# Performance work log

Hardware: AMD Instinct MI355X
Metric: run time of the kernel (lower is better)

Reference implementation:

```python
import jax, jax.numpy as jnp
import numpy as np

D_MODEL = 1024
NUM_HEADS = 16
D_K = D_MODEL // NUM_HEADS


def setup_inputs() -> dict:
    key = jax.random.key(0)
    ks = jax.random.split(key, 9)
    s = 1.0 / np.sqrt(D_MODEL)
    x = jax.random.normal(ks[0], (4, 2048, D_MODEL), dtype=jnp.float32)
    Wq = jax.random.uniform(ks[1], (D_MODEL, D_MODEL), jnp.float32, -s, s)
    bq = jax.random.uniform(ks[2], (D_MODEL,), jnp.float32, -s, s)
    Wk = jax.random.uniform(ks[3], (D_MODEL, D_MODEL), jnp.float32, -s, s)
    bk = jax.random.uniform(ks[4], (D_MODEL,), jnp.float32, -s, s)
    Wv = jax.random.uniform(ks[5], (D_MODEL, D_MODEL), jnp.float32, -s, s)
    bv = jax.random.uniform(ks[6], (D_MODEL,), jnp.float32, -s, s)
    Wo = jax.random.uniform(ks[7], (D_MODEL, D_MODEL), jnp.float32, -s, s)
    bo = jax.random.uniform(ks[8], (D_MODEL,), jnp.float32, -s, s)
    return {"x": x, "Wq": Wq, "bq": bq, "Wk": Wk, "bk": bk,
            "Wv": Wv, "bv": bv, "Wo": Wo, "bo": bo}


def reference(x, Wq, bq, Wk, bk, Wv, bv, Wo, bo):
    B, S, _ = x.shape
    # Linear projections (torch Linear: x @ W.T + b)
    q = x @ Wq.T + bq
    k = x @ Wk.T + bk
    v = x @ Wv.T + bv
    # [B, H, S, d_k]
    q = q.reshape(B, S, NUM_HEADS, D_K).transpose(0, 2, 1, 3)
    k = k.reshape(B, S, NUM_HEADS, D_K).transpose(0, 2, 1, 3)
    v = v.reshape(B, S, NUM_HEADS, D_K).transpose(0, 2, 1, 3)
    score = jnp.einsum('bhqd,bhkd->bhqk', q, k) / jnp.sqrt(jnp.float32(D_K))
    causal = jnp.tril(jnp.ones((S, S), dtype=bool))  # True = keep
    score = jnp.where(causal[None, None], score, -jnp.inf)
    attn = jax.nn.softmax(score, axis=-1)
    out = jnp.einsum('bhqk,bhkd->bhqd', attn, v)
    out = out.transpose(0, 2, 1, 3).reshape(B, S, D_MODEL)
    return out @ Wo.T + bo
```

## Files before the change

kernel.cpp:

```cpp
#include <hip/hip_runtime.h>
#include <hip/hip_bf16.h>
#include <stdint.h>

#define D_MODEL 1024
#define SEQ     2048
#define BATCH   4
#define NHEAD   16
#define DKH     64
#define MTOT    (BATCH * SEQ)

typedef __bf16 bf16x8 __attribute__((ext_vector_type(8)));
typedef __bf16 bf16x4 __attribute__((ext_vector_type(4)));
typedef float  floatx4 __attribute__((ext_vector_type(4)));
typedef short  s16x4  __attribute__((ext_vector_type(4)));

#define GLOAD_LDS16(gp, lp)                                            \
    __builtin_amdgcn_global_load_lds(                                  \
        (const __attribute__((address_space(1))) unsigned int*)(gp),   \
        (__attribute__((address_space(3))) unsigned int*)(lp), 16, 0, 0)

#define MFMA16(a, b, c) __builtin_amdgcn_mfma_f32_16x16x32_bf16(a, b, c, 0, 0, 0)

#if __has_builtin(__builtin_amdgcn_exp2f)
#define EXP2(x) __builtin_amdgcn_exp2f(x)
#else
#define EXP2(x) exp2f(x)
#endif

static __device__ __forceinline__ floatx4 pv_mfma(s16x4 a, s16x4 b, floatx4 c)
{
#if __has_builtin(__builtin_amdgcn_mfma_f32_16x16x16bf16_1k)
    return __builtin_amdgcn_mfma_f32_16x16x16bf16_1k(a, b, c, 0, 0, 0);
#else
    asm("v_mfma_f32_16x16x16_bf16 %0, %1, %2, %0" : "+v"(c) : "v"(a), "v"(b));
    return c;
#endif
}

__global__ __launch_bounds__(256)
void cvt_x_kernel(const float* __restrict__ src, __bf16* __restrict__ dst)
{
    const int i = (blockIdx.x * 256 + threadIdx.x) * 4;
    floatx4 v = *(const floatx4*)(src + i);
    bf16x4 o;
    o[0] = (__bf16)v[0]; o[1] = (__bf16)v[1]; o[2] = (__bf16)v[2]; o[3] = (__bf16)v[3];
    *(bf16x4*)(dst + i) = o;
}

__global__ __launch_bounds__(256)
void cvt_w3_kernel(const float* __restrict__ Wq, const float* __restrict__ Wk,
                   const float* __restrict__ Wv, __bf16* __restrict__ Wcat)
{
    const int z = blockIdx.y;
    const float* src = (z == 0) ? Wq : ((z == 1) ? Wk : Wv);
    const int i = (blockIdx.x * 256 + threadIdx.x) * 4;
    floatx4 v = *(const floatx4*)(src + i);
    bf16x4 o;
    o[0] = (__bf16)v[0]; o[1] = (__bf16)v[1]; o[2] = (__bf16)v[2]; o[3] = (__bf16)v[3];
    *(bf16x4*)(Wcat + (size_t)z * (D_MODEL * D_MODEL) + i) = o;
}

__global__ __launch_bounds__(256)
void qkv_gemm_kernel(const __bf16* __restrict__ xb, const __bf16* __restrict__ Wcat,
                     const float* __restrict__ bq, const float* __restrict__ bk,
                     const float* __restrict__ bv,
                     __bf16* __restrict__ Q, __bf16* __restrict__ K,
                     __bf16* __restrict__ Vt)
{
    __shared__ __align__(16) char smem_raw[128 * 136 * 2];
    __bf16* As = (__bf16*)smem_raw;
    __bf16* Bs = (__bf16*)(smem_raw + 8192);
    __bf16* Cs = (__bf16*)smem_raw;

    const int t    = threadIdx.x;
    const int w    = t >> 6, l = t & 63, quad = l >> 4, r16 = l & 15;
    const int wm   = w & 1, wn = w >> 1;
    const int m0   = blockIdx.y * 128;
    const int n0   = blockIdx.x * 128;
    const int z    = n0 >> 10;
    const float* bias = (z == 0) ? bq : ((z == 1) ? bk : bv);
    __bf16* outQK     = (z == 0) ? Q  : K;
    const float scale = (z == 0) ? 0.18033688011112042f : 1.0f;

    floatx4 acc[4][4];
#pragma unroll
    for (int i = 0; i < 4; ++i)
#pragma unroll
        for (int j = 0; j < 4; ++j) acc[i][j] = (floatx4){0.f, 0.f, 0.f, 0.f};

    const int c0 = t, c1 = t + 256;
    const __bf16* Ag0 = xb   + (size_t)(m0 + (c0 >> 2)) * 1024 + (c0 & 3) * 8;
    const __bf16* Ag1 = xb   + (size_t)(m0 + (c1 >> 2)) * 1024 + (c1 & 3) * 8;
    const __bf16* Bg0 = Wcat + (size_t)(n0 + (c0 >> 2)) * 1024 + (c0 & 3) * 8;
    const __bf16* Bg1 = Wcat + (size_t)(n0 + (c1 >> 2)) * 1024 + (c1 & 3) * 8;
    unsigned int* lAs = (unsigned int*)As;
    unsigned int* lBs = (unsigned int*)Bs;

    for (int k0 = 0; k0 < 1024; k0 += 32) {
        __syncthreads();
        GLOAD_LDS16(Ag0 + k0, lAs + c0 * 4);
        GLOAD_LDS16(Ag1 + k0, lAs + c1 * 4);
        GLOAD_LDS16(Bg0 + k0, lBs + c0 * 4);
        GLOAD_LDS16(Bg1 + k0, lBs + c1 * 4);
        __syncthreads();

        bf16x8 af[4], bfm[4];
#pragma unroll
        for (int i = 0; i < 4; ++i)
            af[i] = *(const bf16x8*)&As[(wm * 64 + i * 16 + r16) * 32 + quad * 8];
#pragma unroll
        for (int j = 0; j < 4; ++j)
            bfm[j] = *(const bf16x8*)&Bs[(wn * 64 + j * 16 + r16) * 32 + quad * 8];
#pragma unroll
        for (int i = 0; i < 4; ++i)
#pragma unroll
            for (int j = 0; j < 4; ++j)
                acc[i][j] = MFMA16(af[i], bfm[j], acc[i][j]);
    }

    __syncthreads();

    if (z == 2) {
#pragma unroll
        for (int i = 0; i < 4; ++i) {
            const int mb = wm * 64 + i * 16 + quad * 4;
#pragma unroll
            for (int j = 0; j < 4; ++j) {
                const int nl = wn * 64 + j * 16 + r16;
                const float bb = bias[(n0 + nl) & 1023];
                bf16x4 p4;
#pragma unroll
                for (int r = 0; r < 4; ++r) p4[r] = (__bf16)(acc[i][j][r] + bb);
                *(bf16x4*)&Cs[nl * 136 + mb] = p4;
            }
        }
    } else {
#pragma unroll
        for (int i = 0; i < 4; ++i) {
            const int mb = wm * 64 + i * 16 + quad * 4;
#pragma unroll
            for (int j = 0; j < 4; ++j) {
                const int nl = wn * 64 + j * 16 + r16;
                const float bb = bias[(n0 + nl) & 1023];
#pragma unroll
                for (int r = 0; r < 4; ++r)
                    Cs[(mb + r) * 136 + nl] =
                        (__bf16)((acc[i][j][r] + bb) * scale);
            }
        }
    }
    __syncthreads();

    const int b  = m0 >> 11;
    if (z == 2) {
#pragma unroll
        for (int k = 0; k < 8; ++k) {
            const int nl = (t >> 4) + k * 16;
            const int ml = (t & 15) * 8;
            bf16x8 row = *(const bf16x8*)&Cs[nl * 136 + ml];
            const int f = (n0 + nl) & 1023, h = f >> 6, d = f & 63;
            const int s = (m0 & 2047) + ml;
            *(bf16x8*)&Vt[((size_t)((b * 16 + h) * 64 + d) << 11) + s] = row;
        }
    } else {
#pragma unroll
        for (int k = 0; k < 8; ++k) {
            const int ml = (t >> 4) + k * 16;
            const int nl = (t & 15) * 8;
            bf16x8 row = *(const bf16x8*)&Cs[ml * 136 + nl];
            const int f = (n0 + nl) & 1023, h = f >> 6, d = f & 63;
            const int s = (m0 & 2047) + ml;
            *(bf16x8*)&outQK[((size_t)(b * 16 + h) << 17) + ((size_t)s << 6) + d]
                = row;
        }
    }
}

__global__ __launch_bounds__(256)
void out_gemm_kernel(const __bf16* __restrict__ A, const __bf16* __restrict__ Wob,
                     const float* __restrict__ bo, float* __restrict__ out)
{
    __shared__ __align__(16) __bf16 As[128 * 32];
    __shared__ __align__(16) __bf16 Bs[128 * 32];

    const int t    = threadIdx.x;
    const int w    = t >> 6, l = t & 63, quad = l >> 4, r16 = l & 15;
    const int wm   = w & 1, wn = w >> 1;
    const int m0   = blockIdx.y * 128;
    const int n0   = blockIdx.x * 128;

    floatx4 acc[4][4];
#pragma unroll
    for (int i = 0; i < 4; ++i)
#pragma unroll
        for (int j = 0; j < 4; ++j) acc[i][j] = (floatx4){0.f, 0.f, 0.f, 0.f};

    const int c0 = t, c1 = t + 256;
    const __bf16* Ag0 = A   + (size_t)(m0 + (c0 >> 2)) * 1024 + (c0 & 3) * 8;
    const __bf16* Ag1 = A   + (size_t)(m0 + (c1 >> 2)) * 1024 + (c1 & 3) * 8;
    const __bf16* Bg0 = Wob + (size_t)(n0 + (c0 >> 2)) * 1024 + (c0 & 3) * 8;
    const __bf16* Bg1 = Wob + (size_t)(n0 + (c1 >> 2)) * 1024 + (c1 & 3) * 8;
    unsigned int* lAs = (unsigned int*)As;
    unsigned int* lBs = (unsigned int*)Bs;

    for (int k0 = 0; k0 < 1024; k0 += 32) {
        __syncthreads();
        GLOAD_LDS16(Ag0 + k0, lAs + c0 * 4);
        GLOAD_LDS16(Ag1 + k0, lAs + c1 * 4);
        GLOAD_LDS16(Bg0 + k0, lBs + c0 * 4);
        GLOAD_LDS16(Bg1 + k0, lBs + c1 * 4);
        __syncthreads();

        bf16x8 af[4], bfm[4];
#pragma unroll
        for (int i = 0; i < 4; ++i)
            af[i] = *(const bf16x8*)&As[(wm * 64 + i * 16 + r16) * 32 + quad * 8];
#pragma unroll
        for (int j = 0; j < 4; ++j)
            bfm[j] = *(const bf16x8*)&Bs[(wn * 64 + j * 16 + r16) * 32 + quad * 8];
#pragma unroll
        for (int i = 0; i < 4; ++i)
#pragma unroll
            for (int j = 0; j < 4; ++j)
                acc[i][j] = MFMA16(af[i], bfm[j], acc[i][j]);
    }

#pragma unroll
    for (int i = 0; i < 4; ++i) {
        const int mg = m0 + wm * 64 + i * 16 + quad * 4;
#pragma unroll
        for (int j = 0; j < 4; ++j) {
            const int ng = n0 + wn * 64 + j * 16 + r16;
            const float bb = bo[ng];
#pragma unroll
            for (int r = 0; r < 4; ++r)
                out[(size_t)(mg + r) * 1024 + ng] = acc[i][j][r] + bb;
        }
    }
}

__global__ __launch_bounds__(256, 4)
void attn_kernel(const __bf16* __restrict__ Qg, const __bf16* __restrict__ Kg,
                 const __bf16* __restrict__ Vtg, __bf16* __restrict__ O)
{
    __shared__ __align__(16) __bf16 Ks[2][64 * 72];
    __shared__ __align__(16) __bf16 Vs[2][64 * 72];

    const int t    = threadIdx.x;
    const int w    = t >> 6, l = t & 63, quad = l >> 4, r16 = l & 15;
    const int bh   = blockIdx.x;
    const int y    = blockIdx.y;
    const int p    = y >> 1, half = y & 1;
    const int qa   = 15 - p, qb = p;
    const size_t base = (size_t)bh * SEQ * DKH;
    const int d0   = 2 * qa + half;
    const int d1   = 2 * qb + half;
    const int nkt  = d0 + 1;
    const int row0 = qa * 128 + half * 64 + w * 16;
    const int row1 = qb * 128 + half * 64 + w * 16;

    const s16x4 ones16 = {(short)0x3F80, (short)0x3F80,
                          (short)0x3F80, (short)0x3F80};

    bf16x8 qf00, qf01, qf10, qf11;
    qf00 = *(const bf16x8*)&Qg[base + (size_t)(row0 + r16) * 64 + quad * 8];
    qf01 = *(const bf16x8*)&Qg[base + (size_t)(row0 + r16) * 64 + 32 + quad * 8];
    qf10 = *(const bf16x8*)&Qg[base + (size_t)(row1 + r16) * 64 + quad * 8];
    qf11 = *(const bf16x8*)&Qg[base + (size_t)(row1 + r16) * 64 + 32 + quad * 8];

    floatx4 o[2][4];
#pragma unroll
    for (int mi = 0; mi < 2; ++mi)
#pragma unroll
        for (int j = 0; j < 4; ++j) o[mi][j] = (floatx4){0.f, 0.f, 0.f, 0.f};
    floatx4 osum[2];
    osum[0] = (floatx4){0.f, 0.f, 0.f, 0.f};
    osum[1] = (floatx4){0.f, 0.f, 0.f, 0.f};

    const int srow = t >> 3;
    const int sg   = (t & 7) * 8;

    bf16x8 kc0, kc1, vc0, vc1;
    kc0 = *(const bf16x8*)&Kg[base + (size_t)srow * 64 + sg];
    kc1 = *(const bf16x8*)&Kg[base + (size_t)(32 + srow) * 64 + sg];
    vc0 = *(const bf16x8*)&Vtg[base + (size_t)srow * 2048 + sg];
    vc1 = *(const bf16x8*)&Vtg[base + (size_t)(32 + srow) * 2048 + sg];

    for (int kt = 0; kt < nkt; ++kt) {
        __bf16* ks = Ks[kt & 1];
        __bf16* vs = Vs[kt & 1];
        *(bf16x8*)&ks[srow * 72 + sg] = kc0;
        *(bf16x8*)&ks[(32 + srow) * 72 + sg] = kc1;
        *(bf16x8*)&vs[srow * 72 + sg] = vc0;
        *(bf16x8*)&vs[(32 + srow) * 72 + sg] = vc1;
        if (kt + 1 < nkt) {
            const int kr = (kt + 1) * 64;
            kc0 = *(const bf16x8*)&Kg[base + (size_t)(kr + srow) * 64 + sg];
            kc1 = *(const bf16x8*)&Kg[base + (size_t)(kr + 32 + srow) * 64 + sg];
            vc0 = *(const bf16x8*)&Vtg[base + (size_t)srow * 2048 + kr + sg];
            vc1 = *(const bf16x8*)&Vtg[base + (size_t)(32 + srow) * 2048 + kr + sg];
        }
        __syncthreads();

        const bool a1 = (kt <= d1);
        __builtin_amdgcn_s_setprio(1);
        bf16x8 kf0, kf1;
#pragma unroll
        for (int j = 0; j < 4; ++j) {
            kf0 = *(const bf16x8*)&ks[(j * 16 + r16) * 72 + quad * 8];
            kf1 = *(const bf16x8*)&ks[(j * 16 + r16) * 72 + 32 + quad * 8];
            floatx4 z0 = (floatx4){0.f, 0.f, 0.f, 0.f};
            floatx4 z1 = (floatx4){0.f, 0.f, 0.f, 0.f};
            z0 = MFMA16(kf0, qf00, z0);
            z0 = MFMA16(kf1, qf01, z0);
            if (a1) {
                z1 = MFMA16(kf0, qf10, z1);
                z1 = MFMA16(kf1, qf11, z1);
            }
            const int kg = kt * 64 + j * 16 + quad * 4;
            bf16x4 pb0, pb1;
            if (kt < d0) {
#pragma unroll
                for (int r = 0; r < 4; ++r)
                    pb0[r] = (__bf16)EXP2(z0[r]);
            } else {
                const int qg0 = row0 + r16;
#pragma unroll
                for (int r = 0; r < 4; ++r) {
                    float pp = 0.f;
                    if (kg + r <= qg0) pp = EXP2(z0[r]);
                    pb0[r] = (__bf16)pp;
                }
            }
            s16x4 pa0 = __builtin_bit_cast(s16x4, pb0);
            s16x4 pa1;
            if (a1) {
                if (kt < d1) {
#pragma unroll
                    for (int r = 0; r < 4; ++r)
                        pb1[r] = (__bf16)EXP2(z1[r]);
                } else {
                    const int qg1 = row1 + r16;
#pragma unroll
                    for (int r = 0; r < 4; ++r) {
                        float pp = 0.f;
                        if (kg + r <= qg1) pp = EXP2(z1[r]);
                        pb1[r] = (__bf16)pp;
                    }
                }
                pa1 = __builtin_bit_cast(s16x4, pb1);
            }
            osum[0] = pv_mfma(pa0, ones16, osum[0]);
            if (a1) osum[1] = pv_mfma(pa1, ones16, osum[1]);
#pragma unroll
            for (int jd = 0; jd < 4; ++jd) {
                const s16x4 vv =
                    *(const s16x4*)&vs[(jd * 16 + r16) * 72 + j * 16 + quad * 4];
                o[0][jd] = pv_mfma(pa0, vv, o[0][jd]);
                if (a1) o[1][jd] = pv_mfma(pa1, vv, o[1][jd]);
            }
        }
        __builtin_amdgcn_s_setprio(0);
    }

    const int b = bh >> 4, h = bh & 15;
#pragma unroll
    for (int mi = 0; mi < 2; ++mi) {
        const int rowb = (mi == 0) ? row0 : row1;
#pragma unroll
        for (int r = 0; r < 4; ++r) {
            const int qrow = rowb + quad * 4 + r;
            const float inv = 1.f / osum[mi][r];
#pragma unroll
            for (int jd = 0; jd < 4; ++jd) {
                const int d = jd * 16 + r16;
                O[((size_t)(b * SEQ + qrow) * D_MODEL) + h * 64 + d] =
                    (__bf16)(o[mi][jd][r] * inv);
            }
        }
    }
}

extern "C" void kernel_launch(void* const* d_in, const int* in_sizes, int n_in,
                              void* d_out, int out_size, void* d_ws, size_t ws_size,
                              hipStream_t stream)
{
    (void)in_sizes; (void)n_in; (void)out_size; (void)ws_size;
    const float* x  = (const float*)d_in[0];
    const float* Wq = (const float*)d_in[1];
    const float* bq = (const float*)d_in[2];
    const float* Wk = (const float*)d_in[3];
    const float* bk = (const float*)d_in[4];
    const float* Wv = (const float*)d_in[5];
    const float* bv = (const float*)d_in[6];
    const float* Wo = (const float*)d_in[7];
    const float* bo = (const float*)d_in[8];
    float* out = (float*)d_out;

    const size_t n_elem = (size_t)MTOT * D_MODEL;
    const int    w_n    = D_MODEL * D_MODEL;
    __bf16* Qb  = (__bf16*)d_out;
    __bf16* xb  = Qb + n_elem;
    __bf16* Kb   = (__bf16*)d_ws;
    __bf16* Vtb  = Kb + n_elem;
    __bf16* Ab   = Vtb + n_elem;
    __bf16* Wcat = Ab;
    __bf16* Wob  = Kb;

    cvt_x_kernel<<<MTOT * D_MODEL / 1024, 256, 0, stream>>>(x, xb);
    cvt_w3_kernel<<<dim3(w_n / 1024, 3), 256, 0, stream>>>(Wq, Wk, Wv, Wcat);
    qkv_gemm_kernel<<<dim3(24, 64), 256, 0, stream>>>(xb, Wcat, bq, bk, bv,
                                                      Qb, Kb, Vtb);
    attn_kernel<<<dim3(64, 16), 256, 0, stream>>>(Qb, Kb, Vtb, Ab);
    cvt_x_kernel<<<w_n / 1024, 256, 0, stream>>>(Wo, Wob);
    out_gemm_kernel<<<dim3(8, 64), 256, 0, stream>>>(Ab, Wob, bo, out);
}
```

Measured before the change: 253.0 us.

## Swizzle GEMM LDS layout, merge conversion kernels, shrink out-GEMM M tile

Applies an XOR swizzle to the 16-byte chunks that global_load_lds writes into LDS in both GEMMs. Fragment reads use the matching swizzled offset, which is meant to reduce LDS bank conflicts. The x and Wq/Wk/Wv fp32-to-bf16 conversions are merged into one launch to save launch overhead. The output GEMM tile shrinks from 128x128 to 64x128, doubling the block count to fill more CUs, at the cost of less reuse of each B tile.

```diff
diff --git a/kernel.cpp b/kernel.cpp
--- a/kernel.cpp
+++ b/kernel.cpp
@@ -38,6 +38,30 @@
 }
 
 __global__ __launch_bounds__(256)
+void cvt_pre_kernel(const float* __restrict__ x, const float* __restrict__ Wq,
+                    const float* __restrict__ Wk, const float* __restrict__ Wv,
+                    __bf16* __restrict__ xb, __bf16* __restrict__ Wcat)
+{
+    int bid = blockIdx.x;
+    const float* src;
+    __bf16* dst;
+    if (bid < 8192) {
+        src = x;  dst = xb;
+    } else {
+        bid -= 8192;
+        const int z = bid >> 10;
+        bid &= 1023;
+        src = (z == 0) ? Wq : ((z == 1) ? Wk : Wv);
+        dst = Wcat + (size_t)z * (D_MODEL * D_MODEL);
+    }
+    const int i = (bid * 256 + threadIdx.x) * 4;
+    floatx4 v = *(const floatx4*)(src + i);
+    bf16x4 o;
+    o[0] = (__bf16)v[0]; o[1] = (__bf16)v[1]; o[2] = (__bf16)v[2]; o[3] = (__bf16)v[3];
+    *(bf16x4*)(dst + i) = o;
+}
+
+__global__ __launch_bounds__(256)
 void cvt_x_kernel(const float* __restrict__ src, __bf16* __restrict__ dst)
 {
     const int i = (blockIdx.x * 256 + threadIdx.x) * 4;
@@ -45,19 +69,6 @@
     bf16x4 o;
     o[0] = (__bf16)v[0]; o[1] = (__bf16)v[1]; o[2] = (__bf16)v[2]; o[3] = (__bf16)v[3];
     *(bf16x4*)(dst + i) = o;
-}
-
-__global__ __launch_bounds__(256)
-void cvt_w3_kernel(const float* __restrict__ Wq, const float* __restrict__ Wk,
-                   const float* __restrict__ Wv, __bf16* __restrict__ Wcat)
-{
-    const int z = blockIdx.y;
-    const float* src = (z == 0) ? Wq : ((z == 1) ? Wk : Wv);
-    const int i = (blockIdx.x * 256 + threadIdx.x) * 4;
-    floatx4 v = *(const floatx4*)(src + i);
-    bf16x4 o;
-    o[0] = (__bf16)v[0]; o[1] = (__bf16)v[1]; o[2] = (__bf16)v[2]; o[3] = (__bf16)v[3];
-    *(bf16x4*)(Wcat + (size_t)z * (D_MODEL * D_MODEL) + i) = o;
 }
 
 __global__ __launch_bounds__(256)
@@ -89,12 +100,16 @@
         for (int j = 0; j < 4; ++j) acc[i][j] = (floatx4){0.f, 0.f, 0.f, 0.f};
 
     const int c0 = t, c1 = t + 256;
-    const __bf16* Ag0 = xb   + (size_t)(m0 + (c0 >> 2)) * 1024 + (c0 & 3) * 8;
-    const __bf16* Ag1 = xb   + (size_t)(m0 + (c1 >> 2)) * 1024 + (c1 & 3) * 8;
-    const __bf16* Bg0 = Wcat + (size_t)(n0 + (c0 >> 2)) * 1024 + (c0 & 3) * 8;
-    const __bf16* Bg1 = Wcat + (size_t)(n0 + (c1 >> 2)) * 1024 + (c1 & 3) * 8;
+    const int row0 = c0 >> 2, s0 = ((c0 & 3) ^ (row0 & 3)) * 8;
+    const int row1 = c1 >> 2, s1 = ((c1 & 3) ^ (row1 & 3)) * 8;
+    const __bf16* Ag0 = xb   + (size_t)(m0 + row0) * 1024 + s0;
+    const __bf16* Ag1 = xb   + (size_t)(m0 + row1) * 1024 + s1;
+    const __bf16* Bg0 = Wcat + (size_t)(n0 + row0) * 1024 + s0;
+    const __bf16* Bg1 = Wcat + (size_t)(n0 + row1) * 1024 + s1;
     unsigned int* lAs = (unsigned int*)As;
     unsigned int* lBs = (unsigned int*)Bs;
+
+    const int fsw = (quad ^ (r16 & 3)) * 8;
 
     for (int k0 = 0; k0 < 1024; k0 += 32) {
         __syncthreads();
@@ -107,10 +122,10 @@
         bf16x8 af[4], bfm[4];
 #pragma unroll
         for (int i = 0; i < 4; ++i)
-            af[i] = *(const bf16x8*)&As[(wm * 64 + i * 16 + r16) * 32 + quad * 8];
+            af[i] = *(const bf16x8*)&As[(wm * 64 + i * 16 + r16) * 32 + fsw];
 #pragma unroll
         for (int j = 0; j < 4; ++j)
-            bfm[j] = *(const bf16x8*)&Bs[(wn * 64 + j * 16 + r16) * 32 + quad * 8];
+            bfm[j] = *(const bf16x8*)&Bs[(wn * 64 + j * 16 + r16) * 32 + fsw];
 #pragma unroll
         for (int i = 0; i < 4; ++i)
 #pragma unroll
@@ -180,54 +195,58 @@
 void out_gemm_kernel(const __bf16* __restrict__ A, const __bf16* __restrict__ Wob,
                      const float* __restrict__ bo, float* __restrict__ out)
 {
-    __shared__ __align__(16) __bf16 As[128 * 32];
+    __shared__ __align__(16) __bf16 As[64 * 32];
     __shared__ __align__(16) __bf16 Bs[128 * 32];
 
     const int t    = threadIdx.x;
     const int w    = t >> 6, l = t & 63, quad = l >> 4, r16 = l & 15;
     const int wm   = w & 1, wn = w >> 1;
-    const int m0   = blockIdx.y * 128;
+    const int m0   = blockIdx.y * 64;
     const int n0   = blockIdx.x * 128;
 
-    floatx4 acc[4][4];
-#pragma unroll
-    for (int i = 0; i < 4; ++i)
+    floatx4 acc[2][4];
+#pragma unroll
+    for (int i = 0; i < 2; ++i)
 #pragma unroll
         for (int j = 0; j < 4; ++j) acc[i][j] = (floatx4){0.f, 0.f, 0.f, 0.f};
 
-    const int c0 = t, c1 = t + 256;
-    const __bf16* Ag0 = A   + (size_t)(m0 + (c0 >> 2)) * 1024 + (c0 & 3) * 8;
-    const __bf16* Ag1 = A   + (size_t)(m0 + (c1 >> 2)) * 1024 + (c1 & 3) * 8;
-    const __bf16* Bg0 = Wob + (size_t)(n0 + (c0 >> 2)) * 1024 + (c0 & 3) * 8;
-    const __bf16* Bg1 = Wob + (size_t)(n0 + (c1 >> 2)) * 1024 + (c1 & 3) * 8;
+    const int ca  = t;
+    const int ra  = ca >> 2, sa = ((ca & 3) ^ (ra & 3)) * 8;
+    const int cb0 = t, cb1 = t + 256;
+    const int rb0 = cb0 >> 2, sb0 = ((cb0 & 3) ^ (rb0 & 3)) * 8;
+    const int rb1 = cb1 >> 2, sb1 = ((cb1 & 3) ^ (rb1 & 3)) * 8;
+    const __bf16* Ag  = A   + (size_t)(m0 + ra) * 1024 + sa;
+    const __bf16* Bg0 = Wob + (size_t)(n0 + rb0) * 1024 + sb0;
+    const __bf16* Bg1 = Wob + (size_t)(n0 + rb1) * 1024 + sb1;
     unsigned int* lAs = (unsigned int*)As;
     unsigned int* lBs = (unsigned int*)Bs;
 
+    const int fsw = (quad ^ (r16 & 3)) * 8;
+
     for (int k0 = 0; k0 < 1024; k0 += 32) {
         __syncthreads();
-        GLOAD_LDS16(Ag0 + k0, lAs + c0 * 4);
-        GLOAD_LDS16(Ag1 + k0, lAs + c1 * 4);
-        GLOAD_LDS16(Bg0 + k0, lBs + c0 * 4);
-        GLOAD_LDS16(Bg1 + k0, lBs + c1 * 4);
+        GLOAD_LDS16(Ag  + k0, lAs + ca * 4);
+        GLOAD_LDS16(Bg0 + k0, lBs + cb0 * 4);
+        GLOAD_LDS16(Bg1 + k0, lBs + cb1 * 4);
         __syncthreads();
 
-        bf16x8 af[4], bfm[4];
-#pragma unroll
-        for (int i = 0; i < 4; ++i)
-            af[i] = *(const bf16x8*)&As[(wm * 64 + i * 16 + r16) * 32 + quad * 8];
+        bf16x8 af[2], bfm[4];
+#pragma unroll
+        for (int i = 0; i < 2; ++i)
+            af[i] = *(const bf16x8*)&As[(wm * 32 + i * 16 + r16) * 32 + fsw];
 #pragma unroll
         for (int j = 0; j < 4; ++j)
-            bfm[j] = *(const bf16x8*)&Bs[(wn * 64 + j * 16 + r16) * 32 + quad * 8];
-#pragma unroll
-        for (int i = 0; i < 4; ++i)
+            bfm[j] = *(const bf16x8*)&Bs[(wn * 64 + j * 16 + r16) * 32 + fsw];
+#pragma unroll
+        for (int i = 0; i < 2; ++i)
 #pragma unroll
             for (int j = 0; j < 4; ++j)
                 acc[i][j] = MFMA16(af[i], bfm[j], acc[i][j]);
     }
 
 #pragma unroll
-    for (int i = 0; i < 4; ++i) {
-        const int mg = m0 + wm * 64 + i * 16 + quad * 4;
+    for (int i = 0; i < 2; ++i) {
+        const int mg = m0 + wm * 32 + i * 16 + quad * 4;
 #pragma unroll
         for (int j = 0; j < 4; ++j) {
             const int ng = n0 + wn * 64 + j * 16 + r16;
@@ -407,11 +426,10 @@
     __bf16* Wcat = Ab;
     __bf16* Wob  = Kb;
 
-    cvt_x_kernel<<<MTOT * D_MODEL / 1024, 256, 0, stream>>>(x, xb);
-    cvt_w3_kernel<<<dim3(w_n / 1024, 3), 256, 0, stream>>>(Wq, Wk, Wv, Wcat);
+    cvt_pre_kernel<<<8192 + 3072, 256, 0, stream>>>(x, Wq, Wk, Wv, xb, Wcat);
     qkv_gemm_kernel<<<dim3(24, 64), 256, 0, stream>>>(xb, Wcat, bq, bk, bv,
                                                       Qb, Kb, Vtb);
     attn_kernel<<<dim3(64, 16), 256, 0, stream>>>(Qb, Kb, Vtb, Ab);
     cvt_x_kernel<<<w_n / 1024, 256, 0, stream>>>(Wo, Wob);
-    out_gemm_kernel<<<dim3(8, 64), 256, 0, stream>>>(Ab, Wob, bo, out);
-}
+    out_gemm_kernel<<<dim3(8, 128), 256, 0, stream>>>(Ab, Wob, bo, out);
+}
```

After: 255.2 us. No clear change (+0.9%).
